# Kernel tuning notes

Measured on AMD Instinct MI355X. Metric: run time of the kernel, lower is better.

The kernel has to match this reference:

```python
import math
import jax, jax.numpy as jnp
import numpy as np

H, N, L, B = 768, 64, 2048, 4
DT_MIN, DT_MAX = 1e-3, 1e-1


def setup_inputs() -> dict:
    key = jax.random.key(0)
    ks = jax.random.split(key, 7)
    # s4d_lin eigenvalue init: Re(lambda) = -0.5, Im(lambda) = pi*n
    log_neg_real = jnp.full((H, N), math.log(0.5), dtype=jnp.float32)
    imag = math.pi * jnp.broadcast_to(jnp.arange(N, dtype=jnp.float32)[None, :], (H, N))
    B_re = jax.random.normal(ks[0], (H, N), dtype=jnp.float32) * 0.5
    B_im = jax.random.normal(ks[1], (H, N), dtype=jnp.float32) * 0.5
    C_re = jax.random.normal(ks[2], (H, N), dtype=jnp.float32) * 0.5
    C_im = jax.random.normal(ks[3], (H, N), dtype=jnp.float32) * 0.5
    log_dt = jax.random.uniform(ks[4], (H,), dtype=jnp.float32) * (math.log(DT_MAX) - math.log(DT_MIN)) + math.log(DT_MIN)
    D = jax.random.normal(ks[5], (H,), dtype=jnp.float32) * 0.01
    u = jax.random.normal(ks[6], (B, H, L), dtype=jnp.float32)
    return {"u": u, "log_neg_real": log_neg_real, "imag": imag,
            "B_re": B_re, "B_im": B_im, "C_re": C_re, "C_im": C_im,
            "log_dt": log_dt, "D": D}


def reference(u, log_neg_real, imag, B_re, B_im, C_re, C_im, log_dt, D):
    Lseq = u.shape[-1]
    # eigenvalues with guaranteed Re < 0
    Lambda = -jnp.exp(log_neg_real) + 1j * imag              # (H, N) complex
    dt = jnp.exp(log_dt)[:, None]                            # (H, 1)
    # ZOH discretization
    A_bar = jnp.exp(Lambda * dt)                             # (H, N)
    B_bar = (A_bar - 1.0) * (1.0 / Lambda) * (B_re + 1j * B_im)
    C = C_re + 1j * C_im
    # Vandermonde kernel: K[h, l] = Re( sum_n C*B_bar * A_bar^l )
    powers = jnp.arange(Lseq, dtype=jnp.float32)             # (L,)
    A_powers = jnp.exp(jnp.log(A_bar)[:, :, None] * powers[None, None, :])  # (H, N, L)
    K = jnp.sum((C * B_bar)[:, :, None] * A_powers, axis=1).real            # (H, L)
    # causal conv via FFT with 2L zero-padding
    fft_len = 2 * Lseq
    u_f = jnp.fft.rfft(u, n=fft_len, axis=-1)                # (B, H, fft/2+1)
    K_f = jnp.fft.rfft(K, n=fft_len, axis=-1)                # (H, fft/2+1)
    y = jnp.fft.irfft(u_f * K_f[None], n=fft_len, axis=-1)[..., :Lseq]
    return y + D[None, :, None] * u
```

## Files before the change

kernel.cpp:

```cpp
#include <hip/hip_runtime.h>

#define HH 768
#define NN 64
#define LL 2048
#define BB 4

typedef __attribute__((ext_vector_type(2))) float f32x2;

#define UF_OFF  0
#define WRE_OFF 8704
#define WIM_OFF 26112
#define SZ_OFF  34560
#define KP_OFF  51200
#define AB_OFF  51712
#define CB_OFF  52224
#define POOL_SZ 52736

__device__ __forceinline__ float2 cmul(float2 a, float2 b) {
    return make_float2(fmaf(a.x, b.x, -(a.y * b.y)), fmaf(a.x, b.y, a.y * b.x));
}
__device__ __forceinline__ unsigned short f2bf(float x) {
    union { float f; unsigned u; } v; v.f = x;
    return (unsigned short)((v.u + 0x7fffu + ((v.u >> 16) & 1u)) >> 16);
}
__device__ __forceinline__ float lo2f(unsigned v) {
    union { unsigned u; float f; } x; x.u = v << 16; return x.f;
}
__device__ __forceinline__ float hi2f(unsigned v) {
    union { unsigned u; float f; } x; x.u = v & 0xffff0000u; return x.f;
}
__device__ __forceinline__ f32x2 pkfma(f32x2 a, f32x2 b, f32x2 c) {
    return __builtin_elementwise_fma(a, b, c);
}
__device__ __forceinline__ f32x2 splat2(float x) { return (f32x2){x, x}; }
__device__ __forceinline__ f32x2 swapneg(f32x2 v) { return (f32x2){-v[1], v[0]}; }
__device__ __forceinline__ f32x2 cmul2(f32x2 a, f32x2 b) {
    return pkfma(splat2(a[0]), b, splat2(a[1]) * swapneg(b));
}

__global__ __launch_bounds__(256, 3) void ssm_kernel7(
    const float* __restrict__ ug,
    const float* __restrict__ lnr,
    const float* __restrict__ img,
    const float* __restrict__ Brp,
    const float* __restrict__ Bip,
    const float* __restrict__ Crp,
    const float* __restrict__ Cip,
    const float* __restrict__ ldt,
    const float* __restrict__ Dp,
    float* __restrict__ outg)
{
    __shared__ __align__(16) unsigned char POOL[POOL_SZ];
    float*        UF   = (float*)(POOL + UF_OFF);
    float*        WRE  = (float*)(POOL + WRE_OFF);
    unsigned int* WIM  = (unsigned int*)(POOL + WIM_OFF);
    float*        SZ   = (float*)(POOL + SZ_OFF);
    float*        kpad = (float*)(POOL + KP_OFF);
    float2*       Abar = (float2*)(POOL + AB_OFF);
    float2*       CBb  = (float2*)(POOL + CB_OFF);

    const int tid = threadIdx.x;
    const int h = blockIdx.x % HH;
    const int b = blockIdx.x / HH;
    const int lane = tid & 63;
    const int w = tid >> 6;

    const float dt = expf(ldt[h]);
    const float Dh = Dp[h];

    if (tid < NN) {
        const int n = tid;
        const float lre = -expf(lnr[h * NN + n]);
        const float lim = img[h * NN + n];
        const float e = expf(lre * dt);
        const float th = lim * dt;
        const float2 A = make_float2(e * cosf(th), e * sinf(th));
        const float den = lre * lre + lim * lim;
        const float2 invL = make_float2(lre / den, -lim / den);
        const float2 am1 = make_float2(A.x - 1.0f, A.y);
        const float2 Bb = cmul(cmul(am1, invL), make_float2(Brp[h*NN+n], Bip[h*NN+n]));
        const float2 CB = cmul(make_float2(Crp[h*NN+n], Cip[h*NN+n]), Bb);
        Abar[n] = A;
        CBb[n] = CB;
        kpad[n] = 0.f;
    }
    {
        const float4* u4g = (const float4*)(ug + (size_t)(b * HH + h) * LL);
        float4* uf4 = (float4*)UF;
        #pragma unroll
        for (int r = 0; r < 2; ++r) {
            const int i = tid + 256 * r;
            uf4[(i >> 4) * 17 + (i & 15)] = u4g[i];
        }
    }
    __syncthreads();

    {
        const float2 A = Abar[lane];
        const float2 a2 = cmul(A, A), a4 = cmul(a2, a2), a8 = cmul(a4, a4), a16 = cmul(a8, a8);
        float2 pw = cmul(CBb[lane], A);
        for (int i = 0; i < w; ++i) pw = cmul(pw, a16);
        unsigned prevlo = 0;
        #pragma unroll
        for (int jj = 0; jj < 16; ++jj) {
            const int j = 16 * w + jj;
            WRE[lane * 68 + j] = pw.x;
            if ((jj & 1) == 0) prevlo = (unsigned)f2bf(pw.y);
            else WIM[lane * 33 + (j >> 1)] = prevlo | ((unsigned)f2bf(pw.y) << 16);
            pw = cmul(pw, A);
        }
    }
    __syncthreads();

    if (w == 0) {
        float acc = 0.f;
        if (lane == 0) {
            for (int n = 0; n < NN; ++n) acc += CBb[n].x;
        } else {
            const float* col = WRE + (lane - 1);
            #pragma unroll 8
            for (int n = 0; n < NN; ++n) acc += col[n * 68];
        }
        kpad[64 + lane] = acc;
    }
    f32x2 Sres[8];
    {
        const float2 Af = Abar[lane];
        const f32x2 A1 = {Af.x, Af.y};
        const f32x2 A2 = cmul2(A1, A1);
        const f32x2 A3 = cmul2(A2, A1);
        const f32x2 A4 = cmul2(A2, A2);
        const f32x2 A8 = cmul2(A4, A4);
        f32x2 P8[8];
        P8[0] = (f32x2){1.f, 0.f};
        #pragma unroll
        for (int k = 1; k < 8; ++k) P8[k] = cmul2(P8[k-1], A8);
        const float4* uf4 = (const float4*)UF;
        #pragma unroll
        for (int k8 = 0; k8 < 8; ++k8) {
            const int c = w + 4 * k8;
            f32x2 sg[8];
            #pragma unroll
            for (int g = 0; g < 8; ++g) {
                const float4 ua = uf4[c * 17 + 2 * g];
                const float4 ub = uf4[c * 17 + 2 * g + 1];
                f32x2 t = A3 * ua.x;
                t = pkfma(A2, splat2(ua.y), t);
                t = pkfma(A1, splat2(ua.z), t);
                t[0] += ua.w;
                f32x2 t2 = A3 * ub.x;
                t2 = pkfma(A2, splat2(ub.y), t2);
                t2 = pkfma(A1, splat2(ub.z), t2);
                t2[0] += ub.w;
                sg[g] = pkfma(splat2(A4[0]), t, pkfma(splat2(A4[1]), swapneg(t), t2));
            }
            f32x2 S = sg[7];
            #pragma unroll
            for (int g = 0; g < 7; ++g)
                S = pkfma(splat2(P8[7-g][0]), sg[g], pkfma(splat2(P8[7-g][1]), swapneg(sg[g]), S));
            Sres[k8] = S;
        }
    }
    #pragma unroll
    for (int k8 = 0; k8 < 8; ++k8) {
        const int c = w + 4 * k8;
        SZ[c * 130 + lane]      = Sres[k8][0];
        SZ[c * 130 + 64 + lane] = Sres[k8][1];
    }
    __syncthreads();

    if (w == 0) {
        const float2 A = Abar[lane];
        const float2 a2 = cmul(A, A), a4 = cmul(a2, a2), a8 = cmul(a4, a4),
                     a16 = cmul(a8, a8), a32 = cmul(a16, a16), a64 = cmul(a32, a32);
        float xr = 0.f, xi = 0.f;
        for (int c = 0; c < 32; ++c) {
            const float sr = SZ[c * 130 + lane];
            const float si = SZ[c * 130 + 64 + lane];
            SZ[c * 130 + lane]      = xr;
            SZ[c * 130 + 64 + lane] = xi;
            const float nxr = fmaf(a64.x, xr, fmaf(-a64.y, xi, sr));
            xi = fmaf(a64.x, xi, fmaf(a64.y, xr, si));
            xr = nxr;
        }
    }
    const int jl = lane & 3;
    const int jt = 4 * w + jl;
    const int c0 = lane >> 2;
    const int c1 = c0 + 16;
    float a00 = 0.f, a01 = 0.f, a02 = 0.f, a03 = 0.f;
    float a10 = 0.f, a11 = 0.f, a12 = 0.f, a13 = 0.f;
    {
        const float4* u4 = (const float4*)UF;
        const float4* kp4 = (const float4*)kpad;
        const int smax = 4 * w + 4;
        #pragma unroll 4
        for (int s4 = 0; s4 < smax; ++s4) {
            const float4 ua = u4[c0 * 17 + s4];
            const float4 ub = u4[c1 * 17 + s4];
            const float4 Av = kp4[15 + jt - s4];
            const float4 Bv = kp4[16 + jt - s4];
            a00 = fmaf(Bv.x, ua.x, a00); a01 = fmaf(Bv.y, ua.x, a01);
            a02 = fmaf(Bv.z, ua.x, a02); a03 = fmaf(Bv.w, ua.x, a03);
            a10 = fmaf(Bv.x, ub.x, a10); a11 = fmaf(Bv.y, ub.x, a11);
            a12 = fmaf(Bv.z, ub.x, a12); a13 = fmaf(Bv.w, ub.x, a13);
            a00 = fmaf(Av.w, ua.y, a00); a01 = fmaf(Bv.x, ua.y, a01);
            a02 = fmaf(Bv.y, ua.y, a02); a03 = fmaf(Bv.z, ua.y, a03);
            a10 = fmaf(Av.w, ub.y, a10); a11 = fmaf(Bv.x, ub.y, a11);
            a12 = fmaf(Bv.y, ub.y, a12); a13 = fmaf(Bv.z, ub.y, a13);
            a00 = fmaf(Av.z, ua.z, a00); a01 = fmaf(Av.w, ua.z, a01);
            a02 = fmaf(Bv.x, ua.z, a02); a03 = fmaf(Bv.y, ua.z, a03);
            a10 = fmaf(Av.z, ub.z, a10); a11 = fmaf(Av.w, ub.z, a11);
            a12 = fmaf(Bv.x, ub.z, a12); a13 = fmaf(Bv.y, ub.z, a13);
            a00 = fmaf(Av.y, ua.w, a00); a01 = fmaf(Av.z, ua.w, a01);
            a02 = fmaf(Av.w, ua.w, a02); a03 = fmaf(Bv.x, ua.w, a03);
            a10 = fmaf(Av.y, ub.w, a10); a11 = fmaf(Av.z, ub.w, a11);
            a12 = fmaf(Av.w, ub.w, a12); a13 = fmaf(Bv.x, ub.w, a13);
        }
    }
    __syncthreads();

    {
        const int j0 = 4 * jt;
        f32x2 r01 = {a00, a01}, r23 = {a02, a03};
        f32x2 s01 = {a10, a11}, s23 = {a12, a13};
        #pragma unroll 4
        for (int n = 0; n < NN; ++n) {
            const float4 wr = *(const float4*)&WRE[n * 68 + j0];
            const unsigned wa = WIM[n * 33 + (j0 >> 1)];
            const unsigned wb = WIM[n * 33 + (j0 >> 1) + 1];
            const float xr0 = SZ[c0 * 130 + n], xi0 = SZ[c0 * 130 + 64 + n];
            const float xr1 = SZ[c1 * 130 + n], xi1 = SZ[c1 * 130 + 64 + n];
            const f32x2 wr01 = {wr.x, wr.y}, wr23 = {wr.z, wr.w};
            const f32x2 wi01 = {lo2f(wa), hi2f(wa)};
            const f32x2 wi23 = {lo2f(wb), hi2f(wb)};
            r01 = pkfma(wr01, splat2(xr0), r01);
            r23 = pkfma(wr23, splat2(xr0), r23);
            s01 = pkfma(wr01, splat2(xr1), s01);
            s23 = pkfma(wr23, splat2(xr1), s23);
            const float nxi0 = -xi0, nxi1 = -xi1;
            r01 = pkfma(wi01, splat2(nxi0), r01);
            r23 = pkfma(wi23, splat2(nxi0), r23);
            s01 = pkfma(wi01, splat2(nxi1), s01);
            s23 = pkfma(wi23, splat2(nxi1), s23);
        }
        const float4* u4 = (const float4*)UF;
        const float4 uA = u4[c0 * 17 + jt];
        const float4 uB = u4[c1 * 17 + jt];
        float* og = outg + (size_t)(b * HH + h) * LL;
        *(float4*)(og + (size_t)c0 * 64 + j0) =
            make_float4(fmaf(Dh, uA.x, r01[0]), fmaf(Dh, uA.y, r01[1]),
                        fmaf(Dh, uA.z, r23[0]), fmaf(Dh, uA.w, r23[1]));
        *(float4*)(og + (size_t)c1 * 64 + j0) =
            make_float4(fmaf(Dh, uB.x, s01[0]), fmaf(Dh, uB.y, s01[1]),
                        fmaf(Dh, uB.z, s23[0]), fmaf(Dh, uB.w, s23[1]));
    }
}

extern "C" void kernel_launch(void* const* d_in, const int* in_sizes, int n_in,
                              void* d_out, int out_size, void* d_ws, size_t ws_size,
                              hipStream_t stream) {
    (void)in_sizes; (void)n_in; (void)out_size; (void)d_ws; (void)ws_size;
    ssm_kernel7<<<dim3(BB * HH), dim3(256), 0, stream>>>(
        (const float*)d_in[0], (const float*)d_in[1], (const float*)d_in[2],
        (const float*)d_in[3], (const float*)d_in[4], (const float*)d_in[5],
        (const float*)d_in[6], (const float*)d_in[7], (const float*)d_in[8],
        (float*)d_out);
}
```

Measured before the change: 153.4 us.

## Move intra-chunk convolution and state-readout to bf16 MFMA with split-precision operands

Replaces the scalar/packed-FMA intra-chunk causal convolution and the chunk-state readout with 16x16x32 bf16 MFMA instructions. To keep accuracy, operands are split into high and low bf16 parts and three MFMAs are issued per product. The state-prefix scan now writes split bf16 terms directly into shared memory. The kernel taps are computed with wave shuffle reductions instead of a separate column-sum pass. This trades FP32 ALU work for matrix-core throughput, at the cost of extra split conversions and possible precision loss from the bf16 imaginary parts.

```diff
diff --git a/kernel.cpp b/kernel.cpp
--- a/kernel.cpp
+++ b/kernel.cpp
@@ -6,15 +6,19 @@
 #define BB 4
 
 typedef __attribute__((ext_vector_type(2))) float f32x2;
-
-#define UF_OFF  0
-#define WRE_OFF 8704
-#define WIM_OFF 26112
-#define SZ_OFF  34560
-#define KP_OFF  51200
-#define AB_OFF  51712
-#define CB_OFF  52224
-#define POOL_SZ 52736
+typedef __attribute__((ext_vector_type(4))) float f32x4;
+typedef __attribute__((ext_vector_type(8))) short bf16x8;
+typedef __attribute__((ext_vector_type(4))) short bf16x4;
+
+#define UF_OFF   0
+#define WRH_OFF  8704
+#define WRL_OFF  17408
+#define WIT_OFF  26112
+#define SZ_OFF   34816
+#define KP_OFF   52224
+#define AB_OFF   52736
+#define CB_OFF   53248
+#define POOL_SZ  53760
 
 __device__ __forceinline__ float2 cmul(float2 a, float2 b) {
     return make_float2(fmaf(a.x, b.x, -(a.y * b.y)), fmaf(a.x, b.y, a.y * b.x));
@@ -23,11 +27,15 @@
     union { float f; unsigned u; } v; v.f = x;
     return (unsigned short)((v.u + 0x7fffu + ((v.u >> 16) & 1u)) >> 16);
 }
-__device__ __forceinline__ float lo2f(unsigned v) {
-    union { unsigned u; float f; } x; x.u = v << 16; return x.f;
-}
-__device__ __forceinline__ float hi2f(unsigned v) {
-    union { unsigned u; float f; } x; x.u = v & 0xffff0000u; return x.f;
+__device__ __forceinline__ unsigned fbits(float x) { union { float f; unsigned u; } v; v.f = x; return v.u; }
+__device__ __forceinline__ float bitsf(unsigned u) { union { unsigned u; float f; } v; v.u = u; return v.f; }
+__device__ __forceinline__ void tsplit(float x, short& h, short& l) {
+    const unsigned bx = fbits(x);
+    const unsigned hu = (bx + 0x7fffu + ((bx >> 16) & 1u)) >> 16;
+    h = (short)hu;
+    const float r = x - bitsf(hu << 16);
+    const unsigned br = fbits(r);
+    l = (short)((br + 0x7fffu + ((br >> 16) & 1u)) >> 16);
 }
 __device__ __forceinline__ f32x2 pkfma(f32x2 a, f32x2 b, f32x2 c) {
     return __builtin_elementwise_fma(a, b, c);
@@ -37,8 +45,29 @@
 __device__ __forceinline__ f32x2 cmul2(f32x2 a, f32x2 b) {
     return pkfma(splat2(a[0]), b, splat2(a[1]) * swapneg(b));
 }
-
-__global__ __launch_bounds__(256, 3) void ssm_kernel7(
+__device__ __forceinline__ f32x4 mm_bf16(bf16x8 a, bf16x8 b, f32x4 c) {
+    return __builtin_amdgcn_mfma_f32_16x16x32_bf16(a, b, c, 0, 0, 0);
+}
+__device__ __forceinline__ bf16x8 ldw8(const short* p) {
+    const bf16x4 a = *(const bf16x4*)p;
+    const bf16x4 b = *(const bf16x4*)(p + 4);
+    return __builtin_shufflevector(a, b, 0, 1, 2, 3, 4, 5, 6, 7);
+}
+__device__ __forceinline__ void split8(const float* p, bf16x8& h8, bf16x8& l8) {
+    const float4 a = *(const float4*)p;
+    const float4 b = *(const float4*)(p + 4);
+    short h, l;
+    tsplit(a.x, h, l); h8[0] = h; l8[0] = l;
+    tsplit(a.y, h, l); h8[1] = h; l8[1] = l;
+    tsplit(a.z, h, l); h8[2] = h; l8[2] = l;
+    tsplit(a.w, h, l); h8[3] = h; l8[3] = l;
+    tsplit(b.x, h, l); h8[4] = h; l8[4] = l;
+    tsplit(b.y, h, l); h8[5] = h; l8[5] = l;
+    tsplit(b.z, h, l); h8[6] = h; l8[6] = l;
+    tsplit(b.w, h, l); h8[7] = h; l8[7] = l;
+}
+
+__global__ __launch_bounds__(256, 3) void ssm_kernel10(
     const float* __restrict__ ug,
     const float* __restrict__ lnr,
     const float* __restrict__ img,
@@ -51,13 +80,13 @@
     float* __restrict__ outg)
 {
     __shared__ __align__(16) unsigned char POOL[POOL_SZ];
-    float*        UF   = (float*)(POOL + UF_OFF);
-    float*        WRE  = (float*)(POOL + WRE_OFF);
-    unsigned int* WIM  = (unsigned int*)(POOL + WIM_OFF);
-    float*        SZ   = (float*)(POOL + SZ_OFF);
-    float*        kpad = (float*)(POOL + KP_OFF);
-    float2*       Abar = (float2*)(POOL + AB_OFF);
-    float2*       CBb  = (float2*)(POOL + CB_OFF);
+    float*  UF   = (float*)(POOL + UF_OFF);
+    short*  WRH  = (short*)(POOL + WRH_OFF);
+    short*  WRL  = (short*)(POOL + WRL_OFF);
+    short*  WIT  = (short*)(POOL + WIT_OFF);
+    float*  kpad = (float*)(POOL + KP_OFF);
+    float2* Abar = (float2*)(POOL + AB_OFF);
+    float2* CBb  = (float2*)(POOL + CB_OFF);
 
     const int tid = threadIdx.x;
     const int h = blockIdx.x % HH;
@@ -83,6 +112,10 @@
         Abar[n] = A;
         CBb[n] = CB;
         kpad[n] = 0.f;
+        float r = CB.x;
+        r += __shfl_xor(r, 1);  r += __shfl_xor(r, 2);  r += __shfl_xor(r, 4);
+        r += __shfl_xor(r, 8);  r += __shfl_xor(r, 16); r += __shfl_xor(r, 32);
+        if (n == 0) kpad[64] = r;
     }
     {
         const float4* u4g = (const float4*)(ug + (size_t)(b * HH + h) * LL);
@@ -100,29 +133,23 @@
         const float2 a2 = cmul(A, A), a4 = cmul(a2, a2), a8 = cmul(a4, a4), a16 = cmul(a8, a8);
         float2 pw = cmul(CBb[lane], A);
         for (int i = 0; i < w; ++i) pw = cmul(pw, a16);
-        unsigned prevlo = 0;
         #pragma unroll
         for (int jj = 0; jj < 16; ++jj) {
             const int j = 16 * w + jj;
-            WRE[lane * 68 + j] = pw.x;
-            if ((jj & 1) == 0) prevlo = (unsigned)f2bf(pw.y);
-            else WIM[lane * 33 + (j >> 1)] = prevlo | ((unsigned)f2bf(pw.y) << 16);
+            short hre, lre2;
+            tsplit(pw.x, hre, lre2);
+            WRH[j * 68 + lane] = hre;
+            WRL[j * 68 + lane] = lre2;
+            WIT[j * 68 + lane] = (short)f2bf(pw.y);
+            float r = pw.x;
+            r += __shfl_xor(r, 1);  r += __shfl_xor(r, 2);  r += __shfl_xor(r, 4);
+            r += __shfl_xor(r, 8);  r += __shfl_xor(r, 16); r += __shfl_xor(r, 32);
+            if (lane == 0 && j < 63) kpad[65 + j] = r;
             pw = cmul(pw, A);
         }
     }
     __syncthreads();
 
-    if (w == 0) {
-        float acc = 0.f;
-        if (lane == 0) {
-            for (int n = 0; n < NN; ++n) acc += CBb[n].x;
-        } else {
-            const float* col = WRE + (lane - 1);
-            #pragma unroll 8
-            for (int n = 0; n < NN; ++n) acc += col[n * 68];
-        }
-        kpad[64 + lane] = acc;
-    }
     f32x2 Sres[8];
     {
         const float2 Af = Abar[lane];
@@ -164,8 +191,9 @@
     #pragma unroll
     for (int k8 = 0; k8 < 8; ++k8) {
         const int c = w + 4 * k8;
-        SZ[c * 130 + lane]      = Sres[k8][0];
-        SZ[c * 130 + 64 + lane] = Sres[k8][1];
+        float* Sf = (float*)(POOL + SZ_OFF + c * 544);
+        Sf[lane]      = Sres[k8][0];
+        Sf[64 + lane] = Sres[k8][1];
     }
     __syncthreads();
 
@@ -174,86 +202,85 @@
         const float2 a2 = cmul(A, A), a4 = cmul(a2, a2), a8 = cmul(a4, a4),
                      a16 = cmul(a8, a8), a32 = cmul(a16, a16), a64 = cmul(a32, a32);
         float xr = 0.f, xi = 0.f;
+        unsigned char* szb = POOL + SZ_OFF;
         for (int c = 0; c < 32; ++c) {
-            const float sr = SZ[c * 130 + lane];
-            const float si = SZ[c * 130 + 64 + lane];
-            SZ[c * 130 + lane]      = xr;
-            SZ[c * 130 + 64 + lane] = xi;
+            float* Sf = (float*)(szb + c * 544);
+            const float sr = Sf[lane];
+            const float si = Sf[64 + lane];
+            asm volatile("s_waitcnt lgkmcnt(0)" ::: "memory");
+            short* XS = (short*)(szb + c * 544);
+            short hh, ll;
+            tsplit(xr, hh, ll);
+            XS[lane]       = hh;
+            XS[64 + lane]  = ll;
+            const float nxi = -xi;
+            tsplit(nxi, hh, ll);
+            XS[128 + lane] = hh;
+            XS[192 + lane] = ll;
             const float nxr = fmaf(a64.x, xr, fmaf(-a64.y, xi, sr));
             xi = fmaf(a64.x, xi, fmaf(a64.y, xr, si));
             xr = nxr;
         }
     }
-    const int jl = lane & 3;
-    const int jt = 4 * w + jl;
-    const int c0 = lane >> 2;
-    const int c1 = c0 + 16;
-    float a00 = 0.f, a01 = 0.f, a02 = 0.f, a03 = 0.f;
-    float a10 = 0.f, a11 = 0.f, a12 = 0.f, a13 = 0.f;
-    {
-        const float4* u4 = (const float4*)UF;
-        const float4* kp4 = (const float4*)kpad;
-        const int smax = 4 * w + 4;
-        #pragma unroll 4
-        for (int s4 = 0; s4 < smax; ++s4) {
-            const float4 ua = u4[c0 * 17 + s4];
-            const float4 ub = u4[c1 * 17 + s4];
-            const float4 Av = kp4[15 + jt - s4];
-            const float4 Bv = kp4[16 + jt - s4];
-            a00 = fmaf(Bv.x, ua.x, a00); a01 = fmaf(Bv.y, ua.x, a01);
-            a02 = fmaf(Bv.z, ua.x, a02); a03 = fmaf(Bv.w, ua.x, a03);
-            a10 = fmaf(Bv.x, ub.x, a10); a11 = fmaf(Bv.y, ub.x, a11);
-            a12 = fmaf(Bv.z, ub.x, a12); a13 = fmaf(Bv.w, ub.x, a13);
-            a00 = fmaf(Av.w, ua.y, a00); a01 = fmaf(Bv.x, ua.y, a01);
-            a02 = fmaf(Bv.y, ua.y, a02); a03 = fmaf(Bv.z, ua.y, a03);
-            a10 = fmaf(Av.w, ub.y, a10); a11 = fmaf(Bv.x, ub.y, a11);
-            a12 = fmaf(Bv.y, ub.y, a12); a13 = fmaf(Bv.z, ub.y, a13);
-            a00 = fmaf(Av.z, ua.z, a00); a01 = fmaf(Av.w, ua.z, a01);
-            a02 = fmaf(Bv.x, ua.z, a02); a03 = fmaf(Bv.y, ua.z, a03);
-            a10 = fmaf(Av.z, ub.z, a10); a11 = fmaf(Av.w, ub.z, a11);
-            a12 = fmaf(Bv.x, ub.z, a12); a13 = fmaf(Bv.y, ub.z, a13);
-            a00 = fmaf(Av.y, ua.w, a00); a01 = fmaf(Av.z, ua.w, a01);
-            a02 = fmaf(Av.w, ua.w, a02); a03 = fmaf(Bv.x, ua.w, a03);
-            a10 = fmaf(Av.y, ub.w, a10); a11 = fmaf(Av.z, ub.w, a11);
-            a12 = fmaf(Av.w, ub.w, a12); a13 = fmaf(Bv.x, ub.w, a13);
-        }
-    }
-    __syncthreads();
-
-    {
-        const int j0 = 4 * jt;
-        f32x2 r01 = {a00, a01}, r23 = {a02, a03};
-        f32x2 s01 = {a10, a11}, s23 = {a12, a13};
-        #pragma unroll 4
-        for (int n = 0; n < NN; ++n) {
-            const float4 wr = *(const float4*)&WRE[n * 68 + j0];
-            const unsigned wa = WIM[n * 33 + (j0 >> 1)];
-            const unsigned wb = WIM[n * 33 + (j0 >> 1) + 1];
-            const float xr0 = SZ[c0 * 130 + n], xi0 = SZ[c0 * 130 + 64 + n];
-            const float xr1 = SZ[c1 * 130 + n], xi1 = SZ[c1 * 130 + 64 + n];
-            const f32x2 wr01 = {wr.x, wr.y}, wr23 = {wr.z, wr.w};
-            const f32x2 wi01 = {lo2f(wa), hi2f(wa)};
-            const f32x2 wi23 = {lo2f(wb), hi2f(wb)};
-            r01 = pkfma(wr01, splat2(xr0), r01);
-            r23 = pkfma(wr23, splat2(xr0), r23);
-            s01 = pkfma(wr01, splat2(xr1), s01);
-            s23 = pkfma(wr23, splat2(xr1), s23);
-            const float nxi0 = -xi0, nxi1 = -xi1;
-            r01 = pkfma(wi01, splat2(nxi0), r01);
-            r23 = pkfma(wi23, splat2(nxi0), r23);
-            s01 = pkfma(wi01, splat2(nxi1), s01);
-            s23 = pkfma(wi23, splat2(nxi1), s23);
-        }
-        const float4* u4 = (const float4*)UF;
-        const float4 uA = u4[c0 * 17 + jt];
-        const float4 uB = u4[c1 * 17 + jt];
+
+    const int g4 = lane >> 4;
+    const int jq = lane & 15;
+    const int jcol = 16 * w + jq;
+    f32x4 acc0 = {0.f, 0.f, 0.f, 0.f};
+    f32x4 acc1 = {0.f, 0.f, 0.f, 0.f};
+    {
+        auto cstep = [&](int ks) {
+            bf16x8 mh, ml;
+            const int kbase = 64 + jcol - 32 * ks - 8 * g4;
+            #pragma unroll
+            for (int i = 0; i < 8; ++i) {
+                short hh, ll; tsplit(kpad[kbase - i], hh, ll);
+                mh[i] = hh; ml[i] = ll;
+            }
+            bf16x8 uh, ul;
+            split8(UF + jq * 68 + 32 * ks + 8 * g4, uh, ul);
+            acc0 = mm_bf16(uh, mh, acc0); acc0 = mm_bf16(uh, ml, acc0); acc0 = mm_bf16(ul, mh, acc0);
+            split8(UF + (16 + jq) * 68 + 32 * ks + 8 * g4, uh, ul);
+            acc1 = mm_bf16(uh, mh, acc1); acc1 = mm_bf16(uh, ml, acc1); acc1 = mm_bf16(ul, mh, acc1);
+        };
+        cstep(0);
+        if (w >= 2) cstep(1);
+    }
+    const short* wrhp = WRH + jcol * 68 + 8 * g4;
+    const short* wrlp = WRL + jcol * 68 + 8 * g4;
+    const short* witp = WIT + jcol * 68 + 8 * g4;
+    const bf16x8 wrh0 = ldw8(wrhp), wrh1 = ldw8(wrhp + 32);
+    const bf16x8 wrl0 = ldw8(wrlp), wrl1 = ldw8(wrlp + 32);
+    const bf16x8 wim0 = ldw8(witp), wim1 = ldw8(witp + 32);
+    __syncthreads();
+
+    {
+        const short* xq = (const short*)(POOL + SZ_OFF) + jq * 272 + 8 * g4;
+        auto bnd = [&](const short* xp, f32x4 acc) -> f32x4 {
+            bf16x8 t;
+            t = *(const bf16x8*)(xp);        acc = mm_bf16(t, wrh0, acc); acc = mm_bf16(t, wrl0, acc);
+            t = *(const bf16x8*)(xp + 64);   acc = mm_bf16(t, wrh0, acc);
+            t = *(const bf16x8*)(xp + 128);  acc = mm_bf16(t, wim0, acc);
+            t = *(const bf16x8*)(xp + 192);  acc = mm_bf16(t, wim0, acc);
+            t = *(const bf16x8*)(xp + 32);   acc = mm_bf16(t, wrh1, acc); acc = mm_bf16(t, wrl1, acc);
+            t = *(const bf16x8*)(xp + 96);   acc = mm_bf16(t, wrh1, acc);
+            t = *(const bf16x8*)(xp + 160);  acc = mm_bf16(t, wim1, acc);
+            t = *(const bf16x8*)(xp + 224);  acc = mm_bf16(t, wim1, acc);
+            return acc;
+        };
+        acc0 = bnd(xq, acc0);
+        acc1 = bnd(xq + 16 * 272, acc1);
+    }
+
+    {
         float* og = outg + (size_t)(b * HH + h) * LL;
-        *(float4*)(og + (size_t)c0 * 64 + j0) =
-            make_float4(fmaf(Dh, uA.x, r01[0]), fmaf(Dh, uA.y, r01[1]),
-                        fmaf(Dh, uA.z, r23[0]), fmaf(Dh, uA.w, r23[1]));
-        *(float4*)(og + (size_t)c1 * 64 + j0) =
-            make_float4(fmaf(Dh, uB.x, s01[0]), fmaf(Dh, uB.y, s01[1]),
-                        fmaf(Dh, uB.z, s23[0]), fmaf(Dh, uB.w, s23[1]));
+        #pragma unroll
+        for (int r = 0; r < 4; ++r) {
+            const int ca = 4 * g4 + r;
+            const int cb = ca + 16;
+            og[ca * 64 + jcol] = fmaf(Dh, UF[ca * 68 + jcol], acc0[r]);
+            og[cb * 64 + jcol] = fmaf(Dh, UF[cb * 68 + jcol], acc1[r]);
+        }
     }
 }
 
@@ -261,7 +288,7 @@
                               void* d_out, int out_size, void* d_ws, size_t ws_size,
                               hipStream_t stream) {
     (void)in_sizes; (void)n_in; (void)out_size; (void)d_ws; (void)ws_size;
-    ssm_kernel7<<<dim3(BB * HH), dim3(256), 0, stream>>>(
+    ssm_kernel10<<<dim3(BB * HH), dim3(256), 0, stream>>>(
         (const float*)d_in[0], (const float*)d_in[1], (const float*)d_in[2],
         (const float*)d_in[3], (const float*)d_in[4], (const float*)d_in[5],
         (const float*)d_in[6], (const float*)d_in[7], (const float*)d_in[8],
```

After: 147.5 us. -3.8%, faster.
